# Optimization experiments

Measured on AMD Instinct MI355X. Metric: run time of the kernel, lower is better.

## Reference

```python
import jax, jax.numpy as jnp
import numpy as np


def setup_inputs() -> dict:
    key = jax.random.key(0)
    kq, kk, kv = jax.random.split(key, 3)
    B, H, N, D = 2, 16, 2048, 128
    q = jax.random.normal(kq, (B, H, N, D), dtype=jnp.float32)
    k = jax.random.normal(kk, (B, H, N, D), dtype=jnp.float32)
    v = jax.random.normal(kv, (B, H, N, D), dtype=jnp.float32)
    return {"q": q, "k": k, "v": v, "num_sink": 4, "window_size": 1024}


def reference(q, k, v, num_sink, window_size):
    # Sink + sliding-window causal attention (single-device path of the SP wrapper).
    # Query i attends to key j iff j <= i AND (j < num_sink OR i - j < window_size).
    B, H, N, D = q.shape
    scale = 1.0 / np.sqrt(D).astype(np.float32)
    i = jnp.arange(N)[:, None]   # query positions
    j = jnp.arange(N)[None, :]   # key positions
    mask = (j <= i) & ((j < num_sink) | ((i - j) < window_size))  # [N, N]
    scores = jnp.einsum('bhid,bhjd->bhij', q, k) * scale          # [B,H,N,N]
    scores = jnp.where(mask, scores, jnp.finfo(scores.dtype).min)
    attn = jax.nn.softmax(scores, axis=-1)
    return jnp.einsum('bhij,bhjd->bhid', attn, v)
```

## Files before the change

### kernel.cpp

```cpp
#include <hip/hip_runtime.h>
#include <stdint.h>

#define NN 2048
#define DD 128
#define BHH 32
#define QT 64
#define KT 64

typedef short v8s __attribute__((ext_vector_type(8)));
typedef short v4s __attribute__((ext_vector_type(4)));
typedef float v4f __attribute__((ext_vector_type(4)));
typedef float v16f __attribute__((ext_vector_type(16)));
typedef unsigned int u32;
typedef u32 u32x2 __attribute__((ext_vector_type(2)));
typedef u32 u32x4 __attribute__((ext_vector_type(4)));

__device__ __forceinline__ unsigned short f2bf(float x) {
  unsigned u = __builtin_bit_cast(unsigned, x);
  u += 0x7fffu + ((u >> 16) & 1u);
  return (unsigned short)(u >> 16);
}

__device__ __forceinline__ u32 pk2(float a, float b) {
  u32 r;
  asm("v_cvt_pk_bf16_f32 %0, %1, %2" : "=v"(r) : "v"(a), "v"(b));
  return r;
}

__device__ __forceinline__ void gl_lds16(const unsigned short* g, unsigned short* l) {
  __builtin_amdgcn_global_load_lds((const unsigned int*)g, (unsigned int*)l, 16, 0, 0);
}

__global__ __launch_bounds__(256) void prep(const float* __restrict__ K, const float* __restrict__ V,
                     unsigned short* __restrict__ Kb, unsigned short* __restrict__ Vt) {
  const int z = blockIdx.z;
  const int tid = threadIdx.x;
  if (z >= BHH) {
    const int bh = z - BHH;
    const int kb32 = blockIdx.y * 32 + blockIdx.x;
    const int m = tid & 31, kc = tid >> 5;
    const float* src = K + ((size_t)bh * NN + kb32 * 32 + m) * DD + kc * 16;
    v4f a0 = *(const v4f*)(src);
    v4f a1 = *(const v4f*)(src + 4);
    v4f a2 = *(const v4f*)(src + 8);
    v4f a3 = *(const v4f*)(src + 12);
    u32x4 w0 = { pk2(a0[0], a0[1]), pk2(a0[2], a0[3]), pk2(a1[0], a1[1]), pk2(a1[2], a1[3]) };
    u32x4 w1 = { pk2(a2[0], a2[1]), pk2(a2[2], a2[3]), pk2(a3[0], a3[1]), pk2(a3[2], a3[3]) };
    unsigned short* base = Kb + (((size_t)bh * 64 + kb32) * 8 + kc) * 512;
    *(u32x4*)(base + (size_t)m * 8) = w0;
    *(u32x4*)(base + (size_t)(32 + m) * 8) = w1;
    return;
  }
  __shared__ __align__(16) unsigned short t[64 * 68];
  const int bh = z;
  const int n0b = blockIdx.x, d0b = blockIdx.y;
  const int c16 = tid & 15, r4 = tid >> 4;
  const float* src = V + ((size_t)bh * NN + n0b * 64 + r4 * 4) * DD + d0b * 64 + c16 * 4;
  v4f f0 = *(const v4f*)(src);
  v4f f1 = *(const v4f*)(src + DD);
  v4f f2 = *(const v4f*)(src + 2 * DD);
  v4f f3 = *(const v4f*)(src + 3 * DD);
#pragma unroll
  for (int j = 0; j < 4; j++) {
    u32x2 w = { pk2(f0[j], f1[j]), pk2(f2[j], f3[j]) };
    *(u32x2*)(t + (c16 * 4 + j) * 68 + r4 * 4) = w;
  }
  __syncthreads();
  unsigned short* Vfb = Vt + (size_t)bh * (512u * 512);
#pragma unroll
  for (int p = 0; p < 2; p++) {
    const int fid = p * 4 + (tid >> 6);
    const int ktl = fid >> 1, ncl = fid & 1;
    const int lane = tid & 63;
    const int dloc = ncl * 32 + (lane & 31);
    const int nloc = ktl * 16 + (lane >> 5) * 8;
    v4s x0 = *(const v4s*)(t + dloc * 68 + nloc);
    v4s x1 = *(const v4s*)(t + dloc * 68 + nloc + 4);
    v8s o = { x0[0], x0[1], x0[2], x0[3], x1[0], x1[1], x1[2], x1[3] };
    const size_t fi = (size_t)(n0b * 4 + ktl) * 4 + (d0b * 2 + ncl);
    *(v8s*)(Vfb + fi * 512 + (size_t)lane * 8) = o;
  }
}

template <bool SPLIT>
__global__ __launch_bounds__(128, 2) void attn(
    const float* __restrict__ Q, const unsigned short* __restrict__ Kb,
    const unsigned short* __restrict__ Vfr,
    const int* __restrict__ nsp, const int* __restrict__ wsp,
    float* __restrict__ O, unsigned short* __restrict__ pB,
    float* __restrict__ lsA, float* __restrict__ lsB) {
  const int ns = nsp[0], win = wsp[0];
  const int x = blockIdx.x;
  int bh, hf = 0, qis[2], njobs;
  if constexpr (SPLIT) {
    const int xcd = x & 7, r = x >> 3;
    bh = xcd + 8 * (r >> 6);
    const int inner = r & 63;
    qis[0] = inner >> 1; qis[1] = 0; hf = inner & 1; njobs = 1;
  } else {
    const int xcd = x & 7, slot = x >> 3;
    bh = xcd + 8 * (slot / 24);
    const int jobid = slot % 24;
    if (jobid < 16) { njobs = 1; qis[0] = 31 - jobid; qis[1] = 0; }
    else { int p = jobid - 16; njobs = 2; qis[0] = 15 - p; qis[1] = p; }
  }

  const int tid = threadIdx.x;
  const int w = tid >> 6;
  const int l = tid & 63;
  const int m = l & 31;
  const int hi = l >> 5;
  const int rbase = 4 * hi;

  __shared__ __align__(16) unsigned short Kl[2][16 * 512];

  const float csc = 0.088388347648318447f * 1.4426950408889634f;

  const unsigned short* Vfb = Vfr + (size_t)bh * (512u * 512);

  auto mkpa = [&](float a0, float a1, float a2, float a3,
                  float b0, float b1, float b2, float b3) -> v8s {
    u32x2 r02 = __builtin_amdgcn_permlane32_swap(pk2(a0, a1), pk2(b0, b1), false, false);
    u32x2 r13 = __builtin_amdgcn_permlane32_swap(pk2(a2, a3), pk2(b2, b3), false, false);
    u32x4 pw = { r02[0], r13[0], r02[1], r13[1] };
    return __builtin_bit_cast(v8s, pw);
  };

  for (int ji = 0; ji < njobs; ji++) {
    const int q0 = qis[ji] * QT;
    const int qrow0w = q0 + w * 32;
    const int qi = qrow0w + m;

    v8s qf[8];
    {
      const float* qb = Q + ((size_t)bh * NN + qi) * DD + hi * 8;
#pragma unroll
      for (int kc = 0; kc < 8; kc++) {
        v4f a = *(const v4f*)(qb + kc * 16);
        v4f b = *(const v4f*)(qb + kc * 16 + 4);
        u32x4 pw = { pk2(a[0] * csc, a[1] * csc), pk2(a[2] * csc, a[3] * csc),
                     pk2(b[0] * csc, b[1] * csc), pk2(b[2] * csc, b[3] * csc) };
        qf[kc] = __builtin_bit_cast(v8s, pw);
      }
    }

    float lsum = 0.f;
    v16f oa[4];
#pragma unroll
    for (int nc = 0; nc < 4; nc++) oa[nc] = (v16f)(0.f);

    const int wstart = q0 - win + 1;
    const bool sink16_all = (wstart > KT - 1) && (ns <= 16);
    const int kb_lo = sink16_all ? ((wstart >> 6) << 6) : 0;
    const int kb_hi = q0 + QT;
    int kb_begin = kb_lo, kb_end = kb_hi;
    bool do_sink = sink16_all;
    if constexpr (SPLIT) {
      const int T = (kb_hi - kb_lo) >> 6;
      const int TA = (T + 1) >> 1;
      if (hf == 0) { kb_end = kb_lo + TA * KT; do_sink = false; }
      else         { kb_begin = kb_lo + TA * KT; }
    }

    auto issueK = [&](int kb, int buf) {
      const unsigned short* src =
          Kb + (((size_t)bh * 64 + (kb >> 5) + w) * 8) * 512 + (size_t)l * 8;
      unsigned short* dst = &Kl[buf][(w * 8) * 512];
#pragma unroll
      for (int i = 0; i < 8; i++)
        gl_lds16(src + (size_t)i * 512, dst + i * 512);
    };

    const bool haveloop = kb_begin < kb_end;
    if (haveloop) issueK(kb_begin, 0);

    if (do_sink) {
      v8s kf0[8];
#pragma unroll
      for (int kc = 0; kc < 8; kc++)
        kf0[kc] = *(const v8s*)(Kb + ((size_t)bh * 64 * 8 + kc) * 512 + (size_t)l * 8);
      v16f s = (v16f)(0.f);
#pragma unroll
      for (int kc = 0; kc < 8; kc++)
        s = __builtin_amdgcn_mfma_f32_32x32x16_bf16(kf0[kc], qf[kc], s, 0, 0, 0);
#pragma unroll
      for (int reg = 0; reg < 16; reg++) {
        const int kj = (reg & 3) + 8 * (reg >> 2) + rbase;
        const bool valid = (kj < ns) && (kj <= qi);
        s[reg] = valid ? __builtin_amdgcn_exp2f(s[reg]) : 0.f;
      }
      lsum += (((s[0] + s[1]) + (s[2] + s[3])) + ((s[4] + s[5]) + (s[6] + s[7])))
            + (((s[8] + s[9]) + (s[10] + s[11])) + ((s[12] + s[13]) + (s[14] + s[15])));
      v8s pa = mkpa(s[0], s[1], s[2], s[3], s[4], s[5], s[6], s[7]);
#pragma unroll
      for (int nc = 0; nc < 4; nc++) {
        v8s vf = *(const v8s*)(Vfb + (size_t)nc * 512 + (size_t)l * 8);
        oa[nc] = __builtin_amdgcn_mfma_f32_32x32x16_bf16(pa, vf, oa[nc], 0, 0, 0);
      }
    }

    if (haveloop) {
      asm volatile("s_waitcnt vmcnt(0)" ::: "memory");
      __syncthreads();
      int cur = 0;
      for (int kb = kb_begin; kb < kb_end; kb += KT) {
        if (kb + KT < kb_end) issueK(kb + KT, cur ^ 1);
        v8s vf[16];
#pragma unroll
        for (int i = 0; i < 16; i++) {
          const int kt = i >> 2, nc = i & 3;
          vf[i] = *(const v8s*)(Vfb + ((size_t)((kb >> 4) + kt) * 4 + nc) * 512 + (size_t)l * 8);
        }

#pragma unroll
        for (int ct = 0; ct < 2; ct++) {
          v16f s = (v16f)(0.f);
          __builtin_amdgcn_s_setprio(1);
#pragma unroll
          for (int kc = 0; kc < 8; kc++) {
            v8s kfr = *(const v8s*)(&Kl[cur][(ct * 8 + kc) * 512 + l * 8]);
            s = __builtin_amdgcn_mfma_f32_32x32x16_bf16(kfr, qf[kc], s, 0, 0, 0);
          }
          __builtin_amdgcn_s_setprio(0);

          const int kbct = kb + ct * 32;
          const bool full = (kbct + 31 <= qrow0w) && (kbct >= qrow0w + 32 - win);
          if (full) {
#pragma unroll
            for (int reg = 0; reg < 16; reg++) s[reg] = __builtin_amdgcn_exp2f(s[reg]);
          } else {
#pragma unroll
            for (int reg = 0; reg < 16; reg++) {
              const int kj = kbct + (reg & 3) + 8 * (reg >> 2) + rbase;
              const bool valid = (kj <= qi) && ((kj < ns) || (qi - kj < win));
              s[reg] = valid ? __builtin_amdgcn_exp2f(s[reg]) : 0.f;
            }
          }
          lsum += (((s[0] + s[1]) + (s[2] + s[3])) + ((s[4] + s[5]) + (s[6] + s[7])))
                + (((s[8] + s[9]) + (s[10] + s[11])) + ((s[12] + s[13]) + (s[14] + s[15])));

          v8s pa0 = mkpa(s[0], s[1], s[2], s[3], s[4], s[5], s[6], s[7]);
          v8s pa1 = mkpa(s[8], s[9], s[10], s[11], s[12], s[13], s[14], s[15]);

          __builtin_amdgcn_s_setprio(1);
#pragma unroll
          for (int ktl = 0; ktl < 2; ktl++) {
            const v8s pf = ktl ? pa1 : pa0;
#pragma unroll
            for (int nc = 0; nc < 4; nc++)
              oa[nc] = __builtin_amdgcn_mfma_f32_32x32x16_bf16(pf, vf[(ct * 2 + ktl) * 4 + nc],
                                                               oa[nc], 0, 0, 0);
          }
          __builtin_amdgcn_s_setprio(0);
        }

        asm volatile("s_waitcnt vmcnt(0)" ::: "memory");
        __syncthreads();
        cur ^= 1;
      }
    }

    float lt = lsum + __shfl_xor(lsum, 32, 64);
    if constexpr (SPLIT) {
      if (hf == 0) {
        float* ob = O + ((size_t)bh * NN + qrow0w) * DD;
#pragma unroll
        for (int reg = 0; reg < 16; reg++) {
          const int row = (reg & 3) + 8 * (reg >> 2) + rbase;
#pragma unroll
          for (int nc = 0; nc < 4; nc++)
            ob[(size_t)row * DD + nc * 32 + m] = oa[nc][reg];
        }
        if (hi == 0) lsA[((size_t)bh << 11) + qrow0w + m] = lt;
      } else {
        unsigned short* pb = pB + ((size_t)bh * NN + qrow0w) * DD;
#pragma unroll
        for (int reg = 0; reg < 16; reg++) {
          const int row = (reg & 3) + 8 * (reg >> 2) + rbase;
#pragma unroll
          for (int nc = 0; nc < 4; nc++)
            pb[(size_t)row * DD + nc * 32 + m] = f2bf(oa[nc][reg]);
        }
        if (hi == 0) lsB[((size_t)bh << 11) + qrow0w + m] = lt;
      }
    } else {
      const float inv = 1.f / lt;
      float* ob = O + ((size_t)bh * NN + qrow0w) * DD;
#pragma unroll
      for (int reg = 0; reg < 16; reg++) {
        const int row = (reg & 3) + 8 * (reg >> 2) + rbase;
        const float iv = __shfl(inv, row, 64);
#pragma unroll
        for (int nc = 0; nc < 4; nc++)
          ob[(size_t)row * DD + nc * 32 + m] = oa[nc][reg] * iv;
      }
    }
  }
}

__global__ __launch_bounds__(256) void merge(float* __restrict__ O,
    const unsigned short* __restrict__ pB, const float* __restrict__ lsA,
    const float* __restrict__ lsB) {
  const int total4 = BHH * NN * DD / 4;
  for (int i = blockIdx.x * 256 + threadIdx.x; i < total4; i += gridDim.x * 256) {
    v4f o = ((const v4f*)O)[i];
    v4s b = ((const v4s*)pB)[i];
    const int row = i >> 5;
    const float inv = 1.f / (lsA[row] + lsB[row]);
    v4f r;
#pragma unroll
    for (int j = 0; j < 4; j++) {
      const float bf = __builtin_bit_cast(float, (u32)((unsigned short)b[j]) << 16);
      r[j] = (o[j] + bf) * inv;
    }
    ((v4f*)O)[i] = r;
  }
}

extern "C" void kernel_launch(void* const* d_in, const int* in_sizes, int n_in,
                              void* d_out, int out_size, void* d_ws, size_t ws_size,
                              hipStream_t stream) {
  const float* q = (const float*)d_in[0];
  const float* k = (const float*)d_in[1];
  const float* v = (const float*)d_in[2];
  const int* nsp = (const int*)d_in[3];
  const int* wsp = (const int*)d_in[4];
  float* out = (float*)d_out;

  const size_t MB16 = 16777216;
  const size_t LS = (size_t)BHH * NN * 4;
  char* ws = (char*)d_ws;
  unsigned short* kfrag = (unsigned short*)ws;
  unsigned short* vfrag = (unsigned short*)(ws + MB16);

  if (ws_size >= 3 * MB16 + 2 * LS) {
    unsigned short* pB = (unsigned short*)(ws + 2 * MB16);
    float* lsA = (float*)(ws + 3 * MB16);
    float* lsB = (float*)(ws + 3 * MB16 + LS);
    prep<<<dim3(32, 2, 2 * BHH), 256, 0, stream>>>(k, v, kfrag, vfrag);
    attn<true><<<2048, 128, 0, stream>>>(q, kfrag, vfrag, nsp, wsp, out, pB, lsA, lsB);
    merge<<<2048, 256, 0, stream>>>(out, pB, lsA, lsB);
  } else {
    prep<<<dim3(32, 2, 2 * BHH), 256, 0, stream>>>(k, v, kfrag, vfrag);
    attn<false><<<BHH * 24, 128, 0, stream>>>(q, kfrag, vfrag, nsp, wsp, out,
                                              nullptr, nullptr, nullptr);
  }
}
```

Measured before the change: 194.2 us.

## Rebalance split-KV work assignment with fixed-size segments and paired short tiles

Reworks the SPLIT path's block-to-work mapping. Each long query tile (16..31) is now split at a fixed 9-tile KV boundary. Short tiles are paired (15-p with p) so the second block handles the long tile's remainder plus a whole short tile, and the partial output not produced for the pair is zero-filled. This cuts the grid from 2048 to 1536 blocks and aims to even out per-block work instead of halving every tile. The cost is extra zero-fill stores and more complex indexing logic.

```diff
diff --git a/kernel.cpp b/kernel.cpp
--- a/kernel.cpp
+++ b/kernel.cpp
@@ -91,26 +91,66 @@
     float* __restrict__ lsA, float* __restrict__ lsB) {
   const int ns = nsp[0], win = wsp[0];
   const int x = blockIdx.x;
-  int bh, hf = 0, qis[2], njobs;
+
+  int bh, h = 0, nseg = 0, zqi = -1;
+  int sqi[2], skb[2], ske[2];
+  bool ssnk[2];
+  auto rangeOf = [&](int tq, int& lo, int& hi, bool& snk) {
+    const int q0 = tq * QT;
+    const int wst = q0 - win + 1;
+    snk = (wst > KT - 1) && (ns <= 16);
+    lo = snk ? ((wst >> 6) << 6) : 0;
+    hi = q0 + QT;
+  };
   if constexpr (SPLIT) {
-    const int xcd = x & 7, r = x >> 3;
-    bh = xcd + 8 * (r >> 6);
-    const int inner = r & 63;
-    qis[0] = inner >> 1; qis[1] = 0; hf = inner & 1; njobs = 1;
+    const int xcd = x & 7, slot = x >> 3;
+    bh = xcd + 8 * (slot / 48);
+    const int j = slot % 48;
+    if (j < 32) {
+      const int tq = 16 + (j >> 1); h = j & 1;
+      int lo, hi; bool snk; rangeOf(tq, lo, hi, snk);
+      int mid = lo + 9 * KT; if (mid > hi) mid = hi;
+      if (h == 0) { sqi[0] = tq; skb[0] = lo;  ske[0] = mid; ssnk[0] = false; nseg = 1; }
+      else        { sqi[0] = tq; skb[0] = mid; ske[0] = hi;  ssnk[0] = snk;   nseg = 1; }
+    } else {
+      const int p = (j - 32) >> 1; h = (j - 32) & 1;
+      const int qa = 15 - p, qb = p;
+      int loa, hia, lob, hib; bool ska, skbb;
+      rangeOf(qa, loa, hia, ska);
+      rangeOf(qb, lob, hib, skbb);
+      int mida = loa + 9 * KT; if (mida > hia) mida = hia;
+      if (h == 0) {
+        sqi[0] = qa; skb[0] = loa; ske[0] = mida; ssnk[0] = ska && (mida == hia);
+        nseg = 1; zqi = qb;
+      } else {
+        nseg = 0;
+        if (mida < hia) { sqi[0] = qa; skb[0] = mida; ske[0] = hia; ssnk[0] = ska; nseg = 1; }
+        else zqi = qa;
+        sqi[nseg] = qb; skb[nseg] = lob; ske[nseg] = hib; ssnk[nseg] = skbb; nseg++;
+      }
+    }
   } else {
     const int xcd = x & 7, slot = x >> 3;
     bh = xcd + 8 * (slot / 24);
-    const int jobid = slot % 24;
-    if (jobid < 16) { njobs = 1; qis[0] = 31 - jobid; qis[1] = 0; }
-    else { int p = jobid - 16; njobs = 2; qis[0] = 15 - p; qis[1] = p; }
+    const int j = slot % 24;
+    if (j < 16) {
+      int lo, hi; bool sk; sqi[0] = 31 - j; rangeOf(sqi[0], lo, hi, sk);
+      skb[0] = lo; ske[0] = hi; ssnk[0] = sk; nseg = 1;
+    } else {
+      const int p = j - 16;
+      int lo, hi; bool sk;
+      sqi[0] = 15 - p; rangeOf(sqi[0], lo, hi, sk); skb[0] = lo; ske[0] = hi; ssnk[0] = sk;
+      sqi[1] = p;      rangeOf(sqi[1], lo, hi, sk); skb[1] = lo; ske[1] = hi; ssnk[1] = sk;
+      nseg = 2;
+    }
   }
 
   const int tid = threadIdx.x;
   const int w = tid >> 6;
   const int l = tid & 63;
   const int m = l & 31;
-  const int hi = l >> 5;
-  const int rbase = 4 * hi;
+  const int hi_ = l >> 5;
+  const int rbase = 4 * hi_;
 
   __shared__ __align__(16) unsigned short Kl[2][16 * 512];
 
@@ -126,14 +166,16 @@
     return __builtin_bit_cast(v8s, pw);
   };
 
-  for (int ji = 0; ji < njobs; ji++) {
-    const int q0 = qis[ji] * QT;
+  for (int si = 0; si < nseg; ++si) {
+    const int q0 = sqi[si] * QT;
+    const int kb_begin = skb[si], kb_end = ske[si];
+    const bool do_sink = ssnk[si];
     const int qrow0w = q0 + w * 32;
-    const int qi = qrow0w + m;
+    const int qlane = qrow0w + m;
 
     v8s qf[8];
     {
-      const float* qb = Q + ((size_t)bh * NN + qi) * DD + hi * 8;
+      const float* qb = Q + ((size_t)bh * NN + qlane) * DD + hi_ * 8;
 #pragma unroll
       for (int kc = 0; kc < 8; kc++) {
         v4f a = *(const v4f*)(qb + kc * 16);
@@ -149,19 +191,6 @@
 #pragma unroll
     for (int nc = 0; nc < 4; nc++) oa[nc] = (v16f)(0.f);
 
-    const int wstart = q0 - win + 1;
-    const bool sink16_all = (wstart > KT - 1) && (ns <= 16);
-    const int kb_lo = sink16_all ? ((wstart >> 6) << 6) : 0;
-    const int kb_hi = q0 + QT;
-    int kb_begin = kb_lo, kb_end = kb_hi;
-    bool do_sink = sink16_all;
-    if constexpr (SPLIT) {
-      const int T = (kb_hi - kb_lo) >> 6;
-      const int TA = (T + 1) >> 1;
-      if (hf == 0) { kb_end = kb_lo + TA * KT; do_sink = false; }
-      else         { kb_begin = kb_lo + TA * KT; }
-    }
-
     auto issueK = [&](int kb, int buf) {
       const unsigned short* src =
           Kb + (((size_t)bh * 64 + (kb >> 5) + w) * 8) * 512 + (size_t)l * 8;
@@ -186,7 +215,7 @@
 #pragma unroll
       for (int reg = 0; reg < 16; reg++) {
         const int kj = (reg & 3) + 8 * (reg >> 2) + rbase;
-        const bool valid = (kj < ns) && (kj <= qi);
+        const bool valid = (kj < ns) && (kj <= qlane);
         s[reg] = valid ? __builtin_amdgcn_exp2f(s[reg]) : 0.f;
       }
       lsum += (((s[0] + s[1]) + (s[2] + s[3])) + ((s[4] + s[5]) + (s[6] + s[7])))
@@ -232,7 +261,7 @@
 #pragma unroll
             for (int reg = 0; reg < 16; reg++) {
               const int kj = kbct + (reg & 3) + 8 * (reg >> 2) + rbase;
-              const bool valid = (kj <= qi) && ((kj < ns) || (qi - kj < win));
+              const bool valid = (kj <= qlane) && ((kj < ns) || (qlane - kj < win));
               s[reg] = valid ? __builtin_amdgcn_exp2f(s[reg]) : 0.f;
             }
           }
@@ -262,7 +291,7 @@
 
     float lt = lsum + __shfl_xor(lsum, 32, 64);
     if constexpr (SPLIT) {
-      if (hf == 0) {
+      if (h == 0) {
         float* ob = O + ((size_t)bh * NN + qrow0w) * DD;
 #pragma unroll
         for (int reg = 0; reg < 16; reg++) {
@@ -271,7 +300,7 @@
           for (int nc = 0; nc < 4; nc++)
             ob[(size_t)row * DD + nc * 32 + m] = oa[nc][reg];
         }
-        if (hi == 0) lsA[((size_t)bh << 11) + qrow0w + m] = lt;
+        if (hi_ == 0) lsA[((size_t)bh << 11) + qrow0w + m] = lt;
       } else {
         unsigned short* pb = pB + ((size_t)bh * NN + qrow0w) * DD;
 #pragma unroll
@@ -281,7 +310,7 @@
           for (int nc = 0; nc < 4; nc++)
             pb[(size_t)row * DD + nc * 32 + m] = f2bf(oa[nc][reg]);
         }
-        if (hi == 0) lsB[((size_t)bh << 11) + qrow0w + m] = lt;
+        if (hi_ == 0) lsB[((size_t)bh << 11) + qrow0w + m] = lt;
       }
     } else {
       const float inv = 1.f / lt;
@@ -293,6 +322,23 @@
 #pragma unroll
         for (int nc = 0; nc < 4; nc++)
           ob[(size_t)row * DD + nc * 32 + m] = oa[nc][reg] * iv;
+      }
+    }
+  }
+
+  if constexpr (SPLIT) {
+    if (zqi >= 0) {
+      const int q0z = zqi * QT;
+      if (h == 0) {
+        float* ob = O + ((size_t)bh * NN + q0z) * DD;
+        const v4f z4 = (v4f)(0.f);
+        for (int i = tid; i < QT * DD / 4; i += 128) ((v4f*)ob)[i] = z4;
+        if (tid < QT) lsA[((size_t)bh << 11) + q0z + tid] = 0.f;
+      } else {
+        unsigned short* pb = pB + ((size_t)bh * NN + q0z) * DD;
+        const v8s z8 = (v8s)(short(0));
+        for (int i = tid; i < QT * DD / 8; i += 128) ((v8s*)pb)[i] = z8;
+        if (tid < QT) lsB[((size_t)bh << 11) + q0z + tid] = 0.f;
       }
     }
   }
@@ -338,7 +384,7 @@
     float* lsA = (float*)(ws + 3 * MB16);
     float* lsB = (float*)(ws + 3 * MB16 + LS);
     prep<<<dim3(32, 2, 2 * BHH), 256, 0, stream>>>(k, v, kfrag, vfrag);
-    attn<true><<<2048, 128, 0, stream>>>(q, kfrag, vfrag, nsp, wsp, out, pB, lsA, lsB);
+    attn<true><<<BHH * 48, 128, 0, stream>>>(q, kfrag, vfrag, nsp, wsp, out, pB, lsA, lsB);
     merge<<<2048, 256, 0, stream>>>(out, pB, lsA, lsB);
   } else {
     prep<<<dim3(32, 2, 2 * BHH), 256, 0, stream>>>(k, v, kfrag, vfrag);
```

Result: slower. 201.4 us (+3.7%).
